# Kernel tuning notes

Hardware: AMD Instinct MI355X
Metric: run time of the kernel (lower is better)

## Reference

```python
import jax, jax.numpy as jnp
import numpy as np

D_MODEL = 1024
N_HEADS = 16
K_TOP = 64
D_HEAD = D_MODEL // N_HEADS


def setup_inputs() -> dict:
    key = jax.random.key(0)
    ks = jax.random.split(key, 9)
    B, L = 8, 4096
    bound = 1.0 / np.sqrt(D_MODEL)  # nn.Linear default init range
    lin = lambda k: jax.random.uniform(k, (D_MODEL, D_MODEL), jnp.float32, -bound, bound)
    vec = lambda k: jax.random.uniform(k, (D_MODEL,), jnp.float32, -bound, bound)
    return {
        "query": jax.random.normal(ks[0], (B, L, D_MODEL), jnp.float32),
        "Wq": lin(ks[1]), "bq": vec(ks[2]),
        "Wk": lin(ks[3]), "bk": vec(ks[4]),
        "Wv": lin(ks[5]), "bv": vec(ks[6]),
        "Wo": lin(ks[7]), "bo": vec(ks[8]),
    }


def reference(query, Wq, bq, Wk, bk, Wv, bv, Wo, bo):
    B, L_q, D = query.shape
    L_k = L_q  # self-attention: key = value = query
    F_q = L_q // 2 + 1
    F_k = L_k // 2 + 1
    k_top = min(K_TOP, F_q)

    def proj(x, W, b):
        # (B, L, D) -> (B, H, L, d_head)
        return (x @ W + b).reshape(B, -1, N_HEADS, D_HEAD).transpose(0, 2, 1, 3)

    q = proj(query, Wq, bq)
    k = proj(query, Wk, bk)
    v = proj(query, Wv, bv)

    q_freq = jnp.fft.rfft(q, axis=2)  # (B, H, F_q, d_head) complex64
    k_freq = jnp.fft.rfft(k, axis=2)
    v_freq = jnp.fft.rfft(v, axis=2)

    # top-k frequency bins by mean spectral magnitude of the query
    q_energy = jnp.abs(q_freq).mean(axis=-1)  # (B, H, F_q)
    _, idx = jax.lax.top_k(q_energy, k_top)   # (B, H, k)
    mapped_idx = jnp.clip(
        jnp.round(idx.astype(jnp.float32) * (F_k - 1) / (F_q - 1)).astype(jnp.int32),
        0, F_k - 1)

    gather = lambda x, i: jnp.take_along_axis(x, i[..., None], axis=2)
    q_top = gather(q_freq, idx)          # (B, H, k, d_head)
    k_top_freq = gather(k_freq, mapped_idx)
    v_top = gather(v_freq, mapped_idx)

    eps = 1e-8
    attn_score = (q_top.real * k_top_freq.real).sum(-1) / (D_HEAD ** 0.5 + eps)
    attn = jax.nn.softmax(attn_score, axis=-1)[..., None]  # (B, H, k, 1)

    # fill spectrum with mean of query spectrum, then scatter attended bins
    q_mean_freq = q_freq.mean(axis=2, keepdims=True)  # (B, H, 1, d_head) complex
    out_freq = jnp.broadcast_to(q_mean_freq, (B, N_HEADS, F_q, D_HEAD))
    src = (attn * v_top.real).astype(out_freq.dtype)  # real -> complex (imag=0)
    bi = jnp.arange(B)[:, None, None]
    hi = jnp.arange(N_HEADS)[None, :, None]
    out_freq = out_freq.at[bi, hi, idx].set(src)

    out_time = jnp.fft.irfft(out_freq, n=L_q, axis=2)  # (B, H, L, d_head)
    out = out_time.transpose(0, 2, 1, 3).reshape(B, L_q, D)
    return out @ Wo + bo
```

## Files before the change

kernel.cpp:

```cpp
#include <hip/hip_runtime.h>
#include <math.h>
#include <stdint.h>


typedef _Float16 f16;
typedef _Float16 f16x4 __attribute__((ext_vector_type(4)));
typedef _Float16 f16x8 __attribute__((ext_vector_type(8)));
typedef float f32x4 __attribute__((ext_vector_type(4)));

#define PI_F 3.14159265358979323846f
#define PADJ(j) ((j) + ((j) >> 3))

__device__ __forceinline__ void gl_lds16(const void* g, void* l) {
  __builtin_amdgcn_global_load_lds((const __attribute__((address_space(1))) void*)g,
                                   (__attribute__((address_space(3))) void*)l, 16, 0, 0);
}

__device__ __forceinline__ float2 cadd(float2 a, float2 b) { return make_float2(a.x + b.x, a.y + b.y); }
__device__ __forceinline__ float2 csub(float2 a, float2 b) { return make_float2(a.x - b.x, a.y - b.y); }
__device__ __forceinline__ float2 cmul(float2 a, float2 b) {
  return make_float2(a.x * b.x - a.y * b.y, a.x * b.y + a.y * b.x);
}
__device__ __forceinline__ float2 cmni(float2 a) { return make_float2(a.y, -a.x); }

template <int NIT>
__device__ __forceinline__ void stgP(const char* g, size_t gstride, int kb, char* lds,
                                     int tid, int w) {
#pragma unroll
  for (int it = 0; it < NIT; ++it) {
    int ls = it * 256 + tid;
    int j = ls >> 3, s = ls & 7;
    int u = s ^ (j & 7);
    int grow = 2 * j + (u >> 2);
    gl_lds16(g + (size_t)grow * gstride + ((u & 3) << 4) + kb, lds + it * 4096 + w * 1024);
  }
}

__device__ __forceinline__ int pofs(int grow, int q) {
  int j = grow >> 1;
  int u = ((grow & 1) << 2) | q;
  return j * 128 + ((u ^ (j & 7)) << 4);
}

__global__ __launch_bounds__(256) void k_tw(float2* __restrict__ twtab, float2* __restrict__ utab) {
  int j = blockIdx.x * 256 + threadIdx.x;
  if (j < 2048) {
    float ang = (float)j * (-6.28318530717958647692f / 2048.0f);
    twtab[j] = make_float2(cosf(ang), sinf(ang));
  } else if (j < 4097) {
    int f = j - 2048;
    float ang = (float)f * (-6.28318530717958647692f / 4096.0f);
    utab[f] = make_float2(cosf(ang), sinf(ang));
  }
}

__global__ __launch_bounds__(256) void k_prep(const float* __restrict__ Wq, const float* __restrict__ Wo,
                                              f16* __restrict__ WqT, f16* __restrict__ WoT) {
  __shared__ float t[32][33];
  const float* src = blockIdx.z ? Wo : Wq;
  f16* dst = blockIdx.z ? WoT : WqT;
  int c0 = blockIdx.x * 32, r0 = blockIdx.y * 32;
  int tx = threadIdx.x, ty = threadIdx.y;
#pragma unroll
  for (int yy = 0; yy < 4; ++yy)
    t[ty + yy * 8][tx] = src[(size_t)(r0 + ty + yy * 8) * 1024 + c0 + tx];
  __syncthreads();
#pragma unroll
  for (int yy = 0; yy < 4; ++yy)
    dst[(size_t)(c0 + ty + yy * 8) * 1024 + r0 + tx] = (f16)t[tx][ty + yy * 8];
}

__global__ __launch_bounds__(256) void k_prep2(const float* __restrict__ Wk, const float* __restrict__ Wv,
                                               f16* __restrict__ WkT, f16* __restrict__ WvT) {
  __shared__ float t[32][33];
  const float* src = blockIdx.z ? Wv : Wk;
  f16* dst = blockIdx.z ? WvT : WkT;
  int c0 = blockIdx.x * 32, r0 = blockIdx.y * 32;
  int tx = threadIdx.x, ty = threadIdx.y;
#pragma unroll
  for (int yy = 0; yy < 4; ++yy)
    t[ty + yy * 8][tx] = src[(size_t)(r0 + ty + yy * 8) * 1024 + c0 + tx];
  __syncthreads();
#pragma unroll
  for (int yy = 0; yy < 4; ++yy)
    dst[(size_t)(c0 + ty + yy * 8) * 1024 + r0 + tx] = (f16)t[tx][ty + yy * 8];
}

__global__ __launch_bounds__(256) void k_t1(const float* __restrict__ X, f16* __restrict__ Xt16) {
  __shared__ float t[64][65];
  int b = blockIdx.z;
  int l0 = blockIdx.x * 64, d0 = blockIdx.y * 64;
  int tid = threadIdx.x;
#pragma unroll
  for (int it = 0; it < 16; ++it) {
    int lr = it * 4 + (tid >> 6);
    t[lr][tid & 63] = X[((size_t)b * 4096 + l0 + lr) * 1024 + d0 + (tid & 63)];
  }
  __syncthreads();
#pragma unroll
  for (int it = 0; it < 4; ++it) {
    int dd = it * 16 + (tid >> 4);
    int lc = (tid & 15) * 4;
    f16x4 v;
    v[0] = (f16)t[lc][dd]; v[1] = (f16)t[lc + 1][dd];
    v[2] = (f16)t[lc + 2][dd]; v[3] = (f16)t[lc + 3][dd];
    *(f16x4*)&Xt16[((size_t)b * 1024 + d0 + dd) * 4096 + l0 + lc] = v;
  }
}

__device__ __forceinline__ void r8_stage(const float2* __restrict__ cur, float2* __restrict__ nxt,
                                         const float2* __restrict__ tw, int tid, int lg) {
  int Ls = 1 << lg;
  int p = tid >> lg, q = tid & (Ls - 1);
  float2 x[8];
#pragma unroll
  for (int u = 0; u < 8; ++u) x[u] = cur[PADJ(tid + 256 * u)];
  float2 s0 = cadd(x[0], x[4]), d0v = csub(x[0], x[4]);
  float2 s1 = cadd(x[2], x[6]), d1v = csub(x[2], x[6]);
  float2 e0 = cadd(s0, s1), e2 = csub(s0, s1);
  float2 md1 = cmni(d1v);
  float2 e1 = cadd(d0v, md1), e3 = csub(d0v, md1);
  float2 t0 = cadd(x[1], x[5]), u0 = csub(x[1], x[5]);
  float2 t1 = cadd(x[3], x[7]), u1 = csub(x[3], x[7]);
  float2 o0 = cadd(t0, t1), o2 = csub(t0, t1);
  float2 mu1 = cmni(u1);
  float2 o1 = cadd(u0, mu1), o3 = csub(u0, mu1);
  const float C8 = 0.70710678118654752440f;
  float2 w1 = make_float2(C8 * (o1.x + o1.y), C8 * (o1.y - o1.x));
  float2 w2 = cmni(o2);
  float2 w3 = make_float2(C8 * (o3.y - o3.x), -C8 * (o3.x + o3.y));
  float2 y[8];
  y[0] = cadd(e0, o0); y[4] = csub(e0, o0);
  y[1] = cadd(e1, w1); y[5] = csub(e1, w1);
  y[2] = cadd(e2, w2); y[6] = csub(e2, w2);
  y[3] = cadd(e3, w3); y[7] = csub(e3, w3);
  int tb = p << lg;
#pragma unroll
  for (int v = 1; v < 8; ++v) y[v] = cmul(y[v], tw[tb * v]);
  int ob = q + (p << (lg + 3));
#pragma unroll
  for (int v = 0; v < 8; ++v) nxt[PADJ(ob + (v << lg))] = y[v];
}

__global__ __launch_bounds__(256) void k_fft(const f16* __restrict__ Xt16,
                                             const float2* __restrict__ twtab,
                                             const float2* __restrict__ utab,
                                             f16* __restrict__ PReU, f16* __restrict__ PImU,
                                             float* __restrict__ sumXf) {
  __shared__ float2 bufA[2304];
  __shared__ float2 bufB[2304];
  __shared__ float redr[256], redi[256];
  int tid = threadIdx.x;
  int blk = blockIdx.x;

  const f16x8* src = (const f16x8*)(Xt16 + (size_t)blk * 4096);
#pragma unroll
  for (int r = 0; r < 2; ++r) {
    int i8 = r * 256 + tid;
    f16x8 v = src[i8];
#pragma unroll
    for (int j = 0; j < 4; ++j)
      bufA[PADJ(4 * i8 + j)] = make_float2((float)v[2 * j], (float)v[2 * j + 1]);
  }
  __syncthreads();
  r8_stage(bufA, bufB, twtab, tid, 0);
  __syncthreads();
  r8_stage(bufB, bufA, twtab, tid, 3);
  __syncthreads();
  r8_stage(bufA, bufB, twtab, tid, 6);
  __syncthreads();
#pragma unroll
  for (int h = 0; h < 2; ++h) {
    int i = (h << 8) + tid;
    float2 a0 = bufB[PADJ(i)], a1 = bufB[PADJ(i + 512)];
    float2 a2 = bufB[PADJ(i + 1024)], a3 = bufB[PADJ(i + 1536)];
    float2 s02 = cadd(a0, a2), d02 = csub(a0, a2);
    float2 s13 = cadd(a1, a3), d13m = cmni(csub(a1, a3));
    bufA[PADJ(i)] = cadd(s02, s13);
    bufA[PADJ(i + 512)] = cadd(d02, d13m);
    bufA[PADJ(i + 1024)] = csub(s02, s13);
    bufA[PADJ(i + 1536)] = csub(d02, d13m);
  }
  __syncthreads();
  float sumr = 0.f, sumi = 0.f;
  size_t obase = (size_t)blk * 2049;
  for (int f = tid; f <= 2048; f += 256) {
    int fz = f & 2047, fm = (2048 - f) & 2047;
    float2 z = bufA[PADJ(fz)], m = bufA[PADJ(fm)];
    float Er = 0.5f * (z.x + m.x), Ei = 0.5f * (z.y - m.y);
    float Or = 0.5f * (z.y + m.y), Oi = -0.5f * (z.x - m.x);
    float2 wv = utab[f];
    float Xr = Er + wv.x * Or - wv.y * Oi;
    float Xi = Ei + wv.x * Oi + wv.y * Or;
    PReU[obase + f] = (f16)Xr;
    PImU[obase + f] = (f16)Xi;
    sumr += Xr; sumi += Xi;
  }
  __syncthreads();
  redr[tid] = sumr; redi[tid] = sumi;
  __syncthreads();
  for (int s = 128; s > 0; s >>= 1) {
    if (tid < s) { redr[tid] += redr[tid + s]; redi[tid] += redi[tid + s]; }
    __syncthreads();
  }
  if (tid == 0) { sumXf[2 * blk] = redr[0]; sumXf[2 * blk + 1] = redi[0]; }
}

__global__ __launch_bounds__(256) void k_C(const float* __restrict__ sumXf, const float* __restrict__ Wq,
                                           const float* __restrict__ bq,
                                           float* __restrict__ Cre, float* __restrict__ Cim) {
  int b = blockIdx.x >> 2;
  int hd = ((blockIdx.x & 3) << 8) + threadIdx.x;
  float accr = 0.f, acci = 0.f;
  for (int dm = 0; dm < 1024; ++dm) {
    float w = Wq[(size_t)dm * 1024 + hd];
    accr += sumXf[2 * (b * 1024 + dm)] * w;
    acci += sumXf[2 * (b * 1024 + dm) + 1] * w;
  }
  Cre[b * 1024 + hd] = (accr + 4096.0f * bq[hd]) * (1.0f / 2049.0f);
  Cim[b * 1024 + hd] = acci * (1.0f / 2049.0f);
}

__global__ __launch_bounds__(256) void k_t2(const f16* __restrict__ PReU, const f16* __restrict__ PImU,
                                            f16* __restrict__ PT) {
  __shared__ f16 t[32][33];
  int z = blockIdx.z;
  int b = z >> 1, pl = z & 1;
  const f16* src = pl ? PImU : PReU;
  int f0 = blockIdx.x * 32, d0 = blockIdx.y * 32;
  int tx = threadIdx.x, ty = threadIdx.y;
#pragma unroll
  for (int yy = 0; yy < 4; ++yy) {
    int ff = f0 + tx;
    t[ty + yy * 8][tx] = (ff < 2049) ? src[(size_t)(b * 1024 + d0 + ty + yy * 8) * 2049 + ff] : (f16)0.f;
  }
  __syncthreads();
#pragma unroll
  for (int yy = 0; yy < 4; ++yy)
    PT[((size_t)b * 4352 + 2 * (f0 + ty + yy * 8) + pl) * 1024 + d0 + tx] = t[tx][ty + yy * 8];
}

__global__ __launch_bounds__(256, 2) void k_energy(const f16* __restrict__ PT, const f16* __restrict__ WqT,
                                                   const float* __restrict__ bq, float* __restrict__ energy) {
  __shared__ __align__(16) char sM[2][24576];
  int tid = threadIdx.x;
  int lane = tid & 63, w = tid >> 6;
  int lin = blockIdx.x;
  int sw = (lin & 7) * 136 + (lin >> 3);
  int bN = sw & 3, Mblk = sw >> 2;
  int wr = w >> 1, wc = w & 1;
  f32x4 acc[4][8];
#pragma unroll
  for (int mf = 0; mf < 4; ++mf)
#pragma unroll
    for (int nf = 0; nf < 8; ++nf) acc[mf][nf] = 0;

  const char* gA0 = (const char*)PT + (size_t)(Mblk * 128) * 2048;
  const char* gB0 = (const char*)WqT + (size_t)(bN * 256) * 2048;
  int r = lane & 15, q = lane >> 4;
  int aofs[4], bofs[8];
#pragma unroll
  for (int mf = 0; mf < 4; ++mf) aofs[mf] = pofs(wr * 64 + mf * 16 + r, q);
#pragma unroll
  for (int nf = 0; nf < 8; ++nf) bofs[nf] = 8192 + pofs(wc * 128 + nf * 16 + r, q);

  char* b0 = &sM[0][0];
  char* b1 = &sM[1][0];
  auto compute = [&](const char* base) {
    f16x8 aF[4], bF[8];
#pragma unroll
    for (int mf = 0; mf < 4; ++mf) aF[mf] = *(const f16x8*)(base + aofs[mf]);
#pragma unroll
    for (int nf = 0; nf < 8; ++nf) bF[nf] = *(const f16x8*)(base + bofs[nf]);
    __builtin_amdgcn_s_setprio(1);
#pragma unroll
    for (int mf = 0; mf < 4; ++mf)
#pragma unroll
      for (int nf = 0; nf < 8; ++nf)
        acc[mf][nf] = __builtin_amdgcn_mfma_f32_16x16x32_f16(aF[mf], bF[nf], acc[mf][nf], 0, 0, 0);
    __builtin_amdgcn_s_setprio(0);
  };

  stgP<2>(gA0, 2048, 0, b0, tid, w);
  stgP<4>(gB0, 2048, 0, b0 + 8192, tid, w);
  for (int t = 0; t < 16; ++t) {
    int kb1 = (2 * t + 1) * 64;
    stgP<2>(gA0, 2048, kb1, b1, tid, w);
    stgP<4>(gB0, 2048, kb1, b1 + 8192, tid, w);
    asm volatile("s_waitcnt vmcnt(6)\ns_barrier" ::: "memory");
    compute(b0);
    asm volatile("s_barrier" ::: "memory");
    if (t < 15) {
      int kb0 = (2 * t + 2) * 64;
      stgP<2>(gA0, 2048, kb0, b0, tid, w);
      stgP<4>(gB0, 2048, kb0, b0 + 8192, tid, w);
      asm volatile("s_waitcnt vmcnt(6)\ns_barrier" ::: "memory");
    } else {
      asm volatile("s_waitcnt vmcnt(0)\ns_barrier" ::: "memory");
    }
    compute(b1);
    asm volatile("s_barrier" ::: "memory");
  }
  int b = Mblk / 34;
  int tIb = Mblk - b * 34;
  int h0 = bN * 4 + wc * 2;
  bool dc0 = (tIb == 0 && wr == 0 && q == 0);
#pragma unroll
  for (int mf = 0; mf < 4; ++mf) {
    float sE0 = 0.f, sO0 = 0.f, sE1 = 0.f, sO1 = 0.f;
#pragma unroll
    for (int nf = 0; nf < 8; ++nf) {
      float re0 = acc[mf][nf][0], im0 = acc[mf][nf][1];
      float re1 = acc[mf][nf][2], im1 = acc[mf][nf][3];
      if (dc0 && mf == 0) re0 += 4096.0f * bq[(h0 + (nf >> 2)) * 64 + (nf & 3) * 16 + r];
      float m0 = sqrtf(re0 * re0 + im0 * im0);
      float m1 = sqrtf(re1 * re1 + im1 * im1);
      if (nf < 4) { sE0 += m0; sO0 += m1; } else { sE1 += m0; sO1 += m1; }
    }
#pragma unroll
    for (int off = 1; off < 16; off <<= 1) {
      sE0 += __shfl_xor(sE0, off);
      sO0 += __shfl_xor(sO0, off);
      sE1 += __shfl_xor(sE1, off);
      sO1 += __shfl_xor(sO1, off);
    }
    if (r == 0) {
      int fp = tIb * 64 + wr * 32 + mf * 8 + (q << 1);
      energy[((size_t)b * 16 + h0) * 2176 + fp] = sE0 * 0.015625f;
      energy[((size_t)b * 16 + h0) * 2176 + fp + 1] = sO0 * 0.015625f;
      energy[((size_t)b * 16 + h0 + 1) * 2176 + fp] = sE1 * 0.015625f;
      energy[((size_t)b * 16 + h0 + 1) * 2176 + fp + 1] = sO1 * 0.015625f;
    }
  }
}

__global__ __launch_bounds__(256) void k_topk(const float* __restrict__ energy, int* __restrict__ idxb) {
  __shared__ float vals[2049];
  __shared__ unsigned long long wbest[4];
  int tid = threadIdx.x, bh = blockIdx.x;
  const float* e = energy + (size_t)bh * 2176;
  for (int i = tid; i < 2049; i += 256) vals[i] = e[i];
  __syncthreads();
  for (int it = 0; it < 64; ++it) {
    unsigned long long best = 0ull;
    for (int f = tid; f < 2049; f += 256) {
      unsigned b32 = __float_as_uint(vals[f]);
      b32 = (b32 & 0x80000000u) ? ~b32 : (b32 | 0x80000000u);
      unsigned long long k = ((unsigned long long)b32 << 12) | (unsigned)(4095 - f);
      best = (k > best) ? k : best;
    }
#pragma unroll
    for (int off = 32; off > 0; off >>= 1) {
      unsigned long long o = __shfl_xor(best, off);
      best = (o > best) ? o : best;
    }
    if ((tid & 63) == 0) wbest[tid >> 6] = best;
    __syncthreads();
    if (tid == 0) {
      unsigned long long b0 = wbest[0] > wbest[1] ? wbest[0] : wbest[1];
      unsigned long long b1 = wbest[2] > wbest[3] ? wbest[2] : wbest[3];
      unsigned long long bb = b0 > b1 ? b0 : b1;
      int f = 4095 - (int)(bb & 4095ull);
      idxb[bh * 64 + it] = f;
      vals[f] = -1.0f;
    }
    __syncthreads();
  }
}

__global__ __launch_bounds__(256) void k_qkv(const f16* __restrict__ PT, const int* __restrict__ idxb,
                                             const f16* __restrict__ WqT, const f16* __restrict__ WkT,
                                             const f16* __restrict__ WvT, float* __restrict__ part) {
  __shared__ __align__(16) f16 sA[64 * 64];
  __shared__ __align__(16) f16 sB[192 * 64];
  __shared__ int fjs[64];
  int tid = threadIdx.x, lane = tid & 63, w = tid >> 6;
  int bh = blockIdx.x, ks = blockIdx.y;
  int b = bh >> 4, h = bh & 15;
  if (tid < 64) fjs[tid] = idxb[bh * 64 + tid];
  __syncthreads();
  f32x4 acc[4][3];
#pragma unroll
  for (int mf = 0; mf < 4; ++mf)
#pragma unroll
    for (int nf = 0; nf < 3; ++nf) acc[mf][nf] = 0;

  int l8 = lane & 7;
  int lr = lane >> 3;
  int swz = (l8 ^ lr) << 4;

  for (int kt = 0; kt < 4; ++kt) {
    int kbyte = ks * 512 + kt * 128;
#pragma unroll
    for (int t = 0; t < 2; ++t) {
      int ia = w * 2 + t;
      int row = ia * 8 + lr;
      const char* src = (const char*)PT + (size_t)(b * 4352 + 2 * fjs[row]) * 2048 + kbyte + swz;
      gl_lds16(src, (char*)sA + ia * 1024);
    }
#pragma unroll
    for (int t = 0; t < 6; ++t) {
      int ib = w * 6 + t;
      int row = ib * 8 + lr;
      const f16* Wt = (row < 64) ? WqT : (row < 128) ? WkT : WvT;
      const char* src = (const char*)Wt + (size_t)(h * 64 + (row & 63)) * 2048 + kbyte + swz;
      gl_lds16(src, (char*)sB + ib * 1024);
    }
    __syncthreads();
#pragma unroll
    for (int kk = 0; kk < 64; kk += 32) {
      int cb = (kk << 1) + ((lane >> 4) << 4);
      int r = lane & 15;
      f16x8 aF[4], bF[3];
#pragma unroll
      for (int mf = 0; mf < 4; ++mf) {
        int row = mf * 16 + r;
        aF[mf] = *(const f16x8*)((const char*)sA + row * 128 + (cb ^ ((row & 7) << 4)));
      }
#pragma unroll
      for (int nf = 0; nf < 3; ++nf) {
        int row = w * 48 + nf * 16 + r;
        bF[nf] = *(const f16x8*)((const char*)sB + row * 128 + (cb ^ ((row & 7) << 4)));
      }
#pragma unroll
      for (int mf = 0; mf < 4; ++mf)
#pragma unroll
        for (int nf = 0; nf < 3; ++nf)
          acc[mf][nf] = __builtin_amdgcn_mfma_f32_16x16x32_f16(aF[mf], bF[nf], acc[mf][nf], 0, 0, 0);
    }
    __syncthreads();
  }
  float* pb = part + (size_t)(ks * 128 + bh) * 12288;
#pragma unroll
  for (int mf = 0; mf < 4; ++mf)
#pragma unroll
    for (int nf = 0; nf < 3; ++nf)
#pragma unroll
      for (int rr = 0; rr < 4; ++rr) {
        int m = mf * 16 + ((lane >> 4) << 2) + rr;
        int n = w * 48 + nf * 16 + (lane & 15);
        pb[m * 192 + n] = acc[mf][nf][rr];
      }
}

__global__ __launch_bounds__(256) void k_attn2(const float* __restrict__ part, const int* __restrict__ idxb,
                                               const float* __restrict__ bq, const float* __restrict__ bk,
                                               const float* __restrict__ bv, const float* __restrict__ Cre,
                                               f16* __restrict__ ampT) {
  __shared__ float sQKV[64][196];
  __shared__ float scores[64], attns[64];
  __shared__ int fjs[64];
  __shared__ int dcrow;
  int tid = threadIdx.x, bh = blockIdx.x;
  int b = bh >> 4, h = bh & 15;
  if (tid == 0) dcrow = -1;
  __syncthreads();
  if (tid < 64) {
    int f = idxb[bh * 64 + tid];
    fjs[tid] = f;
    if (f == 0) dcrow = tid;
  }
  __syncthreads();
  const float4* p0 = (const float4*)(part + (size_t)bh * 12288);
  const size_t s4 = (size_t)128 * 12288 / 4;
#pragma unroll
  for (int it = 0; it < 12; ++it) {
    int e = it * 256 + tid;
    float4 v0 = p0[e], v1 = p0[e + s4], v2 = p0[e + 2 * s4], v3 = p0[e + 3 * s4];
    float4 v;
    v.x = v0.x + v1.x + v2.x + v3.x;
    v.y = v0.y + v1.y + v2.y + v3.y;
    v.z = v0.z + v1.z + v2.z + v3.z;
    v.w = v0.w + v1.w + v2.w + v3.w;
    int m = e / 48, n0 = (e % 48) * 4;
    *(float4*)&sQKV[m][n0] = v;
  }
  __syncthreads();
  if (dcrow >= 0 && tid < 192) {
    const float* bias = (tid < 64) ? bq : (tid < 128) ? bk : bv;
    sQKV[dcrow][tid] += 4096.0f * bias[h * 64 + (tid & 63)];
  }
  __syncthreads();
  {
    int j = tid >> 2, p = tid & 3;
    float s = 0.f;
#pragma unroll
    for (int c = 0; c < 16; ++c) {
      int cc = p * 16 + c;
      s = fmaf(sQKV[j][cc], sQKV[j][64 + cc], s);
    }
    s += __shfl_xor(s, 1);
    s += __shfl_xor(s, 2);
    if (p == 0) scores[j] = s * 0.125f;
  }
  __syncthreads();
  if (tid < 64) {
    float s = scores[tid];
    float m = s;
#pragma unroll
    for (int off = 32; off > 0; off >>= 1) m = fmaxf(m, __shfl_xor(m, off));
    float ev = expf(s - m);
    float sm = ev;
#pragma unroll
    for (int off = 32; off > 0; off >>= 1) sm += __shfl_xor(sm, off);
    attns[tid] = ev / sm;
  }
  __syncthreads();
  {
    int j = tid >> 2, d0 = (tid & 3) * 16;
    float at = attns[j];
    int fj = fjs[j];
    float wj = (fj == 0 || fj == 2048) ? 0.5f : 1.0f;
#pragma unroll
    for (int q4 = 0; q4 < 4; ++q4) {
      float4 c4 = *(const float4*)&Cre[b * 1024 + h * 64 + d0 + q4 * 4];
      float4 vv = *(const float4*)&sQKV[j][128 + d0 + q4 * 4];
      float av0 = wj * (at * vv.x - c4.x);
      float av1 = wj * (at * vv.y - c4.y);
      float av2 = wj * (at * vv.z - c4.z);
      float av3 = wj * (at * vv.w - c4.w);
      f16* o = ampT + (size_t)bh * 4096 + (d0 + q4 * 4) * 64 + j;
      o[0] = (f16)av0; o[64] = (f16)av1; o[128] = (f16)av2; o[192] = (f16)av3;
    }
  }
}

__global__ __launch_bounds__(256) void k_ot(const f16* __restrict__ ampT, const int* __restrict__ idxb,
                                            const float* __restrict__ Cre, const float* __restrict__ Cim,
                                            f16* __restrict__ OT) {
  __shared__ __align__(16) f16 sAmp[64][72];
  __shared__ float gbuf[256];
  __shared__ int fjs[64];
  int tid = threadIdx.x, lane = tid & 63, w = tid >> 6;
  int bh = blockIdx.x >> 4, tch = blockIdx.x & 15;
  int b = bh >> 4, h = bh & 15;
  if (tid < 64) fjs[tid] = idxb[bh * 64 + tid];
  {
    int row = tid >> 2, seg = tid & 3;
    const f16* src = ampT + (size_t)bh * 4096 + row * 64 + seg * 16;
    f16x8 v0 = *(const f16x8*)src;
    f16x8 v1 = *(const f16x8*)(src + 8);
    *(f16x8*)&sAmp[row][seg * 16] = v0;
    *(f16x8*)&sAmp[row][seg * 16 + 8] = v1;
  }
  __syncthreads();
  int r = lane & 15, q = lane >> 4;
  int tbase = tch * 256 + w * 64;
  const float cang = 0.00153398078788564123f;
  f16x8 aF[4][2];
  float ss[4];
#pragma unroll
  for (int mf = 0; mf < 4; ++mf) {
    int t = tbase + mf * 16 + r;
    float s = 0.f;
#pragma unroll
    for (int kk2 = 0; kk2 < 2; ++kk2) {
      f16x8 a;
#pragma unroll
      for (int jj = 0; jj < 8; ++jj) {
        int j = kk2 * 32 + q * 8 + jj;
        int ridx = (fjs[j] * t) & 4095;
        float sn, cs;
        __sincosf((float)ridx * cang, &sn, &cs);
        s += sn;
        a[jj] = (f16)cs;
      }
      aF[mf][kk2] = a;
    }
    ss[mf] = s;
  }
#pragma unroll
  for (int mf = 0; mf < 4; ++mf) {
    ss[mf] += __shfl_xor(ss[mf], 16);
    ss[mf] += __shfl_xor(ss[mf], 32);
  }
  if (q == 0) {
#pragma unroll
    for (int mf = 0; mf < 4; ++mf) {
      int t = tbase + mf * 16 + r;
      float g = ss[mf];
      if (t & 1) {
        int tp = (t <= 2048) ? t : 4096 - t;
        float sg = (t <= 2048) ? 1.f : -1.f;
        float aa = (float)tp * (PI_F / 4096.0f);
        g -= sg * (cosf(aa) / sinf(aa));
      }
      gbuf[w * 64 + mf * 16 + r] = g;
    }
  }
  f16x8 bF[4][2];
#pragma unroll
  for (int nf = 0; nf < 4; ++nf)
#pragma unroll
    for (int kk2 = 0; kk2 < 2; ++kk2)
      bF[nf][kk2] = *(const f16x8*)&sAmp[nf * 16 + r][kk2 * 32 + q * 8];
  f32x4 acc[4][4];
#pragma unroll
  for (int mf = 0; mf < 4; ++mf)
#pragma unroll
    for (int nf = 0; nf < 4; ++nf) acc[mf][nf] = 0;
#pragma unroll
  for (int kk2 = 0; kk2 < 2; ++kk2)
#pragma unroll
    for (int mf = 0; mf < 4; ++mf)
#pragma unroll
      for (int nf = 0; nf < 4; ++nf)
        acc[mf][nf] = __builtin_amdgcn_mfma_f32_16x16x32_f16(aF[mf][kk2], bF[nf][kk2], acc[mf][nf], 0, 0, 0);
  __syncthreads();
  const float s2L = 2.0f / 4096.0f;
#pragma unroll
  for (int nf = 0; nf < 4; ++nf) {
    int d = nf * 16 + r;
    float cim = Cim[b * 1024 + h * 64 + d];
    float cre = Cre[b * 1024 + h * 64 + d];
#pragma unroll
    for (int mf = 0; mf < 4; ++mf) {
#pragma unroll
      for (int rr = 0; rr < 4; ++rr) {
        int ro = mf * 16 + q * 4 + rr;
        int t = tbase + ro;
        float g = gbuf[w * 64 + ro];
        float val = s2L * (acc[mf][nf][rr] + cim * g) + ((t == 0) ? cre : 0.f);
        OT[((size_t)bh * 4096 + t) * 64 + d] = (f16)val;
      }
    }
  }
}

__global__ __launch_bounds__(256, 2) void k_final(const f16* __restrict__ OT, const f16* __restrict__ WoT,
                                                  const float* __restrict__ bo, float* __restrict__ out) {
  __shared__ __align__(16) char sM[2][24576];
  int tid = threadIdx.x, lane = tid & 63, w = tid >> 6;
  int lin = blockIdx.x;
  int sw = (lin & 7) * 128 + (lin >> 3);
  int bN = sw & 3, Mblk = sw >> 2;
  int wr = w >> 1, wc = w & 1;
  f32x4 acc[4][8];
#pragma unroll
  for (int mf = 0; mf < 4; ++mf)
#pragma unroll
    for (int nf = 0; nf < 8; ++nf) acc[mf][nf] = 0;
  int b = Mblk >> 5, t0 = (Mblk & 31) * 128;
  const char* gB0 = (const char*)WoT + (size_t)(bN * 256) * 2048;
  int r = lane & 15, q = lane >> 4;
  int aofs[4], bofs[8];
#pragma unroll
  for (int mf = 0; mf < 4; ++mf) aofs[mf] = pofs(wr * 64 + mf * 16 + r, q);
#pragma unroll
  for (int nf = 0; nf < 8; ++nf) bofs[nf] = 8192 + pofs(wc * 128 + nf * 16 + r, q);
#define GA_HEAD(ks) ((const char*)OT + ((size_t)(b * 16 + ((ks) >> 1)) * 4096 + t0) * 128)

  char* b0 = &sM[0][0];
  char* b1 = &sM[1][0];
  auto compute = [&](const char* base) {
    f16x8 aF[4], bF[8];
#pragma unroll
    for (int mf = 0; mf < 4; ++mf) aF[mf] = *(const f16x8*)(base + aofs[mf]);
#pragma unroll
    for (int nf = 0; nf < 8; ++nf) bF[nf] = *(const f16x8*)(base + bofs[nf]);
    __builtin_amdgcn_s_setprio(1);
#pragma unroll
    for (int mf = 0; mf < 4; ++mf)
#pragma unroll
      for (int nf = 0; nf < 8; ++nf)
        acc[mf][nf] = __builtin_amdgcn_mfma_f32_16x16x32_f16(aF[mf], bF[nf], acc[mf][nf], 0, 0, 0);
    __builtin_amdgcn_s_setprio(0);
  };

  stgP<2>(GA_HEAD(0), 128, 0, b0, tid, w);
  stgP<4>(gB0, 2048, 0, b0 + 8192, tid, w);
  for (int t = 0; t < 16; ++t) {
    int ks1 = 2 * t + 1;
    stgP<2>(GA_HEAD(ks1), 128, (ks1 & 1) * 64, b1, tid, w);
    stgP<4>(gB0, 2048, ks1 * 64, b1 + 8192, tid, w);
    asm volatile("s_waitcnt vmcnt(6)\ns_barrier" ::: "memory");
    compute(b0);
    asm volatile("s_barrier" ::: "memory");
    if (t < 15) {
      int ks0 = 2 * t + 2;
      stgP<2>(GA_HEAD(ks0), 128, (ks0 & 1) * 64, b0, tid, w);
      stgP<4>(gB0, 2048, ks0 * 64, b0 + 8192, tid, w);
      asm volatile("s_waitcnt vmcnt(6)\ns_barrier" ::: "memory");
    } else {
      asm volatile("s_waitcnt vmcnt(0)\ns_barrier" ::: "memory");
    }
    compute(b1);
    asm volatile("s_barrier" ::: "memory");
  }
#undef GA_HEAD
#pragma unroll
  for (int nf = 0; nf < 8; ++nf) {
    int gcol = bN * 256 + wc * 128 + nf * 16 + r;
    float bcol = bo[gcol];
#pragma unroll
    for (int mf = 0; mf < 4; ++mf) {
#pragma unroll
      for (int rr = 0; rr < 4; ++rr) {
        int grow = Mblk * 128 + wr * 64 + mf * 16 + (q << 2) + rr;
        out[(size_t)grow * 1024 + gcol] = acc[mf][nf][rr] + bcol;
      }
    }
  }
}

extern "C" void kernel_launch(void* const* d_in, const int* in_sizes, int n_in,
                              void* d_out, int out_size, void* d_ws, size_t ws_size,
                              hipStream_t stream) {
  const float* X = (const float*)d_in[0];
  const float* Wq = (const float*)d_in[1];
  const float* bq = (const float*)d_in[2];
  const float* Wk = (const float*)d_in[3];
  const float* bk = (const float*)d_in[4];
  const float* Wv = (const float*)d_in[5];
  const float* bv = (const float*)d_in[6];
  const float* Wo = (const float*)d_in[7];
  const float* bo = (const float*)d_in[8];
  float* out = (float*)d_out;

  if (ws_size < 208928768ULL) return;
  char* w = (char*)d_ws;
  f16* Xt16 = (f16*)(w);
  f16* PT = (f16*)(w);
  f16* WkT = (f16*)(w + 71303168);
  f16* WvT = (f16*)(w + 73400320);
  float* part = (float*)(w + 75497472);
  char* R2 = w + 134217728;
  f16* PReU = (f16*)(R2);
  f16* PImU = (f16*)(R2 + 33570816);
  f16* OT = (f16*)(R2);
  char* R3 = R2 + 67141632;
  float* sumXf = (float*)(R3);
  float* Cre = (float*)(R3 + 65536);
  float* Cim = (float*)(R3 + 98304);
  float* energy = (float*)(R3 + 131072);
  int* idxb = (int*)(R3 + 1245184);
  f16* ampT = (f16*)(R3 + 1277952);
  f16* WqT = (f16*)(R3 + 3375104);
  f16* WoT = (f16*)(R3 + 5472256);
  float2* twtab = (float2*)d_out;
  float2* utab = twtab + 2048;

  dim3 b32(32, 8);
  hipLaunchKernelGGL(k_tw, dim3(17), dim3(256), 0, stream, twtab, utab);
  hipLaunchKernelGGL(k_prep, dim3(32, 32, 2), b32, 0, stream, Wq, Wo, WqT, WoT);
  hipLaunchKernelGGL(k_t1, dim3(64, 16, 8), dim3(256), 0, stream, X, Xt16);
  hipLaunchKernelGGL(k_fft, dim3(8192), dim3(256), 0, stream, Xt16, twtab, utab, PReU, PImU, sumXf);
  hipLaunchKernelGGL(k_prep2, dim3(32, 32, 2), b32, 0, stream, Wk, Wv, WkT, WvT);
  hipLaunchKernelGGL(k_C, dim3(32), dim3(256), 0, stream, sumXf, Wq, bq, Cre, Cim);
  hipLaunchKernelGGL(k_t2, dim3(68, 32, 16), b32, 0, stream, PReU, PImU, PT);
  hipLaunchKernelGGL(k_energy, dim3(1088), dim3(256), 0, stream, PT, WqT, bq, energy);
  hipLaunchKernelGGL(k_topk, dim3(128), dim3(256), 0, stream, energy, idxb);
  hipLaunchKernelGGL(k_qkv, dim3(128, 4), dim3(256), 0, stream, PT, idxb, WqT, WkT, WvT, part);
  hipLaunchKernelGGL(k_attn2, dim3(128), dim3(256), 0, stream, part, idxb, bq, bk, bv, Cre, ampT);
  hipLaunchKernelGGL(k_ot, dim3(2048), dim3(256), 0, stream, ampT, idxb, Cre, Cim, OT);
  hipLaunchKernelGGL(k_final, dim3(1024), dim3(256), 0, stream, OT, WoT, bo, out);
}
```

Baseline: 480.5 us.

## Switch energy and output GEMMs to triple-buffered LDS pipeline, drop setprio

Both the energy-projection GEMM and the final output GEMM move from a double-buffered LDS prefetch to a three-stage ring, issuing loads two k-steps ahead and waiting with vmcnt(12). This hides more global-load latency behind MFMA compute. LDS use per block rises from 48KB to 72KB, which may lower occupancy below the two blocks per CU requested by launch bounds. The s_setprio hints around the MFMA loop are also removed.

```diff
diff --git a/kernel.cpp b/kernel.cpp
--- a/kernel.cpp
+++ b/kernel.cpp
@@ -242,7 +242,7 @@
 
 __global__ __launch_bounds__(256, 2) void k_energy(const f16* __restrict__ PT, const f16* __restrict__ WqT,
                                                    const float* __restrict__ bq, float* __restrict__ energy) {
-  __shared__ __align__(16) char sM[2][24576];
+  __shared__ __align__(16) char sM[3][24576];
   int tid = threadIdx.x;
   int lane = tid & 63, w = tid >> 6;
   int lin = blockIdx.x;
@@ -266,40 +266,41 @@
 
   char* b0 = &sM[0][0];
   char* b1 = &sM[1][0];
+  char* b2 = &sM[2][0];
+  auto bptr = [&](int i) -> char* { return (i == 0) ? b0 : (i == 1) ? b1 : b2; };
+  auto stage = [&](int ks, char* buf) {
+    stgP<2>(gA0, 2048, ks * 64, buf, tid, w);
+    stgP<4>(gB0, 2048, ks * 64, buf + 8192, tid, w);
+  };
   auto compute = [&](const char* base) {
     f16x8 aF[4], bF[8];
 #pragma unroll
     for (int mf = 0; mf < 4; ++mf) aF[mf] = *(const f16x8*)(base + aofs[mf]);
 #pragma unroll
     for (int nf = 0; nf < 8; ++nf) bF[nf] = *(const f16x8*)(base + bofs[nf]);
-    __builtin_amdgcn_s_setprio(1);
 #pragma unroll
     for (int mf = 0; mf < 4; ++mf)
 #pragma unroll
       for (int nf = 0; nf < 8; ++nf)
         acc[mf][nf] = __builtin_amdgcn_mfma_f32_16x16x32_f16(aF[mf], bF[nf], acc[mf][nf], 0, 0, 0);
-    __builtin_amdgcn_s_setprio(0);
   };
 
-  stgP<2>(gA0, 2048, 0, b0, tid, w);
-  stgP<4>(gB0, 2048, 0, b0 + 8192, tid, w);
-  for (int t = 0; t < 16; ++t) {
-    int kb1 = (2 * t + 1) * 64;
-    stgP<2>(gA0, 2048, kb1, b1, tid, w);
-    stgP<4>(gB0, 2048, kb1, b1 + 8192, tid, w);
-    asm volatile("s_waitcnt vmcnt(6)\ns_barrier" ::: "memory");
-    compute(b0);
-    asm volatile("s_barrier" ::: "memory");
-    if (t < 15) {
-      int kb0 = (2 * t + 2) * 64;
-      stgP<2>(gA0, 2048, kb0, b0, tid, w);
-      stgP<4>(gB0, 2048, kb0, b0 + 8192, tid, w);
+  stage(0, b0);
+  stage(1, b1);
+  int i0 = 0, i2 = 2;
+  for (int t = 0; t < 32; ++t) {
+    if (t < 30) {
+      stage(t + 2, bptr(i2));
+      asm volatile("s_waitcnt vmcnt(12)\ns_barrier" ::: "memory");
+    } else if (t == 30) {
       asm volatile("s_waitcnt vmcnt(6)\ns_barrier" ::: "memory");
     } else {
       asm volatile("s_waitcnt vmcnt(0)\ns_barrier" ::: "memory");
     }
-    compute(b1);
+    compute(bptr(i0));
     asm volatile("s_barrier" ::: "memory");
+    i0 = (i0 == 2) ? 0 : i0 + 1;
+    i2 = (i2 == 2) ? 0 : i2 + 1;
   }
   int b = Mblk / 34;
   int tIb = Mblk - b * 34;
@@ -629,7 +630,7 @@
 
 __global__ __launch_bounds__(256, 2) void k_final(const f16* __restrict__ OT, const f16* __restrict__ WoT,
                                                   const float* __restrict__ bo, float* __restrict__ out) {
-  __shared__ __align__(16) char sM[2][24576];
+  __shared__ __align__(16) char sM[3][24576];
   int tid = threadIdx.x, lane = tid & 63, w = tid >> 6;
   int lin = blockIdx.x;
   int sw = (lin & 7) * 128 + (lin >> 3);
@@ -648,46 +649,46 @@
   for (int mf = 0; mf < 4; ++mf) aofs[mf] = pofs(wr * 64 + mf * 16 + r, q);
 #pragma unroll
   for (int nf = 0; nf < 8; ++nf) bofs[nf] = 8192 + pofs(wc * 128 + nf * 16 + r, q);
-#define GA_HEAD(ks) ((const char*)OT + ((size_t)(b * 16 + ((ks) >> 1)) * 4096 + t0) * 128)
 
   char* b0 = &sM[0][0];
   char* b1 = &sM[1][0];
+  char* b2 = &sM[2][0];
+  auto bptr = [&](int i) -> char* { return (i == 0) ? b0 : (i == 1) ? b1 : b2; };
+  auto stage = [&](int ks, char* buf) {
+    const char* gA = (const char*)OT + ((size_t)(b * 16 + (ks >> 1)) * 4096 + t0) * 128;
+    stgP<2>(gA, 128, (ks & 1) * 64, buf, tid, w);
+    stgP<4>(gB0, 2048, ks * 64, buf + 8192, tid, w);
+  };
   auto compute = [&](const char* base) {
     f16x8 aF[4], bF[8];
 #pragma unroll
     for (int mf = 0; mf < 4; ++mf) aF[mf] = *(const f16x8*)(base + aofs[mf]);
 #pragma unroll
     for (int nf = 0; nf < 8; ++nf) bF[nf] = *(const f16x8*)(base + bofs[nf]);
-    __builtin_amdgcn_s_setprio(1);
 #pragma unroll
     for (int mf = 0; mf < 4; ++mf)
 #pragma unroll
       for (int nf = 0; nf < 8; ++nf)
         acc[mf][nf] = __builtin_amdgcn_mfma_f32_16x16x32_f16(aF[mf], bF[nf], acc[mf][nf], 0, 0, 0);
-    __builtin_amdgcn_s_setprio(0);
   };
 
-  stgP<2>(GA_HEAD(0), 128, 0, b0, tid, w);
-  stgP<4>(gB0, 2048, 0, b0 + 8192, tid, w);
-  for (int t = 0; t < 16; ++t) {
-    int ks1 = 2 * t + 1;
-    stgP<2>(GA_HEAD(ks1), 128, (ks1 & 1) * 64, b1, tid, w);
-    stgP<4>(gB0, 2048, ks1 * 64, b1 + 8192, tid, w);
-    asm volatile("s_waitcnt vmcnt(6)\ns_barrier" ::: "memory");
-    compute(b0);
-    asm volatile("s_barrier" ::: "memory");
-    if (t < 15) {
-      int ks0 = 2 * t + 2;
-      stgP<2>(GA_HEAD(ks0), 128, (ks0 & 1) * 64, b0, tid, w);
-      stgP<4>(gB0, 2048, ks0 * 64, b0 + 8192, tid, w);
+  stage(0, b0);
+  stage(1, b1);
+  int i0 = 0, i2 = 2;
+  for (int t = 0; t < 32; ++t) {
+    if (t < 30) {
+      stage(t + 2, bptr(i2));
+      asm volatile("s_waitcnt vmcnt(12)\ns_barrier" ::: "memory");
+    } else if (t == 30) {
       asm volatile("s_waitcnt vmcnt(6)\ns_barrier" ::: "memory");
     } else {
       asm volatile("s_waitcnt vmcnt(0)\ns_barrier" ::: "memory");
     }
-    compute(b1);
+    compute(bptr(i0));
     asm volatile("s_barrier" ::: "memory");
-  }
-#undef GA_HEAD
+    i0 = (i0 == 2) ? 0 : i0 + 1;
+    i2 = (i2 == 2) ? 0 : i2 + 1;
+  }
 #pragma unroll
   for (int nf = 0; nf < 8; ++nf) {
     int gcol = bN * 256 + wc * 128 + nf * 16 + r;
```

New measurement: 481.2 us. Within noise of the previous version (+0.1%).
